# Performance work log

Hardware: AMD Instinct MI355X
Metric: run time of the kernel (lower is better)

The kernel has to match this reference:

```python
import jax, jax.numpy as jnp
import numpy as np

B, M, NV, H, D = 32, 64, 65, 960, 480
ROUNDS = 5
SCALE = D ** -0.5


def _self_att(x, m, qw, qb):
    # x: [B, P, Q, C] attention over Q within each (b, p); m: [B, P, Q]
    qkv = x @ qw.T + qb                      # [B,P,Q,3C]
    q, k, v = jnp.split(qkv, 3, axis=-1)
    # torch builds mask@mask^T/C from a C-times repeated mask == outer product of mask values
    am = m[..., :, None] * m[..., None, :]   # [B,P,Q,Q]
    a = jnp.einsum('bpqc,bpkc->bpqk', q, k) * SCALE
    a = jnp.where(am == 0, -10000.0, a)
    a = jax.nn.softmax(a, axis=-1)
    return jnp.einsum('bpqk,bpkc->bpqc', a, v)


def _attn_logits(x, mask, qw, qb):
    # Attention_logits.forward: attend over value axis, then over key axis
    x = _self_att(x, mask, qw, qb)
    x = _self_att(jnp.swapaxes(x, 1, 2), jnp.swapaxes(mask, 1, 2), qw, qb)
    return jnp.swapaxes(x, 1, 2)


def _biaffine(x1, x2, W, lw, lb):
    # torch.nn.Bilinear (no bias) on the MxN outer grid + Linear(cat(x1,x2)) with bias,
    # computed without materializing the repeated [B,M,N,2D] tensor.
    d = x1.shape[-1]
    bil = jnp.einsum('bmi,oij,bnj->bmno', x1, W, x2)
    lin = (x1 @ lw[:, :d].T)[:, :, None, :] + (x2 @ lw[:, d:].T)[:, None, :, :] + lb
    return bil + lin


def _rounds(key, value, km, vm, W, lw, lb, fw, fb, qw, qb):
    # shared structure of type_classifier / single_classifier (rounds=5, max pooling)
    lm = km[:, :, None] * vm[:, None, :]     # [B,M,N]
    logits = None
    for i in range(ROUNDS):
        logits = _biaffine(key, value, W, lw, lb)          # [B,M,N,out]
        if i < ROUNDS - 1:
            logits = logits @ fw.T + fb                    # [B,M,N,D]
            logits = _attn_logits(logits, lm, qw, qb)
            key = key + logits.max(axis=2)                 # max-pool over values
            value = value + logits.max(axis=1)             # max-pool over keys
        else:
            logits = logits * lm[..., None]
    return logits


def setup_inputs() -> dict:
    root = jax.random.key(0)
    ks = list(jax.random.split(root, 40))
    it = iter(ks)
    nrm = lambda sh, s=0.02: (jax.random.normal(next(it), sh, jnp.float32) * s)
    key = jax.random.normal(next(it), (B, M, H), jnp.float32)
    value = jax.random.normal(next(it), (B, NV, H), jnp.float32)
    klen = jax.random.randint(next(it), (B,), 1, M + 1)
    key_mask = (jnp.arange(M)[None, :] < klen[:, None]).astype(jnp.float32)
    vlen = jax.random.randint(next(it), (B,), 1, NV + 1)
    value_mask = (jnp.arange(NV)[None, :] < vlen[:, None]).astype(jnp.float32)
    return dict(
        key=key, value=value, key_mask=key_mask, value_mask=value_mask,
        w_kt=nrm((D, H)), b_kt=nrm((D,)), w_vt=nrm((D, H)), b_vt=nrm((D,)),
        w_km=nrm((D, H)), b_km=nrm((D,)), w_vm=nrm((D, H)), b_vm=nrm((D,)),
        w_ks=nrm((D, H)), b_ks=nrm((D,)), w_vs=nrm((D, H)), b_vs=nrm((D,)),
        bt_W=nrm((3, D, D)), bt_lw=nrm((3, 2 * D)), bt_lb=nrm((3,)),
        bi_W=nrm((2, D, D)), bi_lw=nrm((2, 2 * D)), bi_lb=nrm((2,)),
        w_ffnt=nrm((D, 3)), b_ffnt=nrm((D,)), w_ffn=nrm((D, 2)), b_ffn=nrm((D,)),
        qkvt_w=nrm((3 * D, D)), qkvt_b=nrm((3 * D,)),
        qkv_w=nrm((3 * D, D)), qkv_b=nrm((3 * D,)),
        w_cls=nrm((2, 2 * D)), b_cls=nrm((2,)),
    )


def reference(key, value, key_mask, value_mask,
              w_kt, b_kt, w_vt, b_vt, w_km, b_km, w_vm, b_vm,
              w_ks, b_ks, w_vs, b_vs,
              bt_W, bt_lw, bt_lb, bi_W, bi_lw, bi_lb,
              w_ffnt, b_ffnt, w_ffn, b_ffn,
              qkvt_w, qkvt_b, qkv_w, qkv_b, w_cls, b_cls):
    # --- type classifier ---
    kt = key @ w_kt.T + b_kt
    vt = value @ w_vt.T + b_vt
    type_logits = _rounds(kt, vt, key_mask, value_mask,
                          bt_W, bt_lw, bt_lb, w_ffnt, b_ffnt, qkvt_w, qkvt_b)  # [B,M,NV,3]
    # drop type token from values
    v1 = value[:, 1:, :]
    vm1 = value_mask[:, 1:]
    type_token = jax.nn.softmax(type_logits[:, :, 0], axis=-1)   # [B,M,3]
    key_type = jnp.argmax(type_token, axis=-1)
    type_single = key_type == 1
    # --- multi classifier (masks unused, as in original) ---
    km_f = key @ w_km.T + b_km
    vm_f = v1 @ w_vm.T + b_vm
    multi_logits = ((km_f @ w_cls[:, :D].T)[:, :, None, :]
                    + (vm_f @ w_cls[:, D:].T)[:, None, :, :] + b_cls)  # [B,M,M? -> B,64,64,2]
    # --- single classifier with key mask restricted to single-link keys ---
    km2 = (key_mask.astype(bool) & type_single).astype(key_mask.dtype)
    ks_f = key @ w_ks.T + b_ks
    vs_f = v1 @ w_vs.T + b_vs
    single_logits = _rounds(ks_f, vs_f, km2, vm1,
                            bi_W, bi_lw, bi_lb, w_ffn, b_ffn, qkv_w, qkv_b)  # [B,64,64,2]
    return (type_logits, multi_logits, single_logits)
```

## Files before the change

kernel.cpp:

```cpp
#include <hip/hip_runtime.h>
#include <math.h>

constexpr int NB = 32;
constexpr int NM = 64;
constexpr int NNV = 65;
constexpr int NH = 960;
constexpr int ND = 480;
constexpr float ATT_SCALE = 0.045643546458763842f;

constexpr int OF_Pq = 0;
constexpr int OF_cq = 4320;
constexpr int OF_Q2 = 5760;
constexpr int OF_V2 = OF_Q2 + 2*1440;
constexpr int OF_dq = 10080;
constexpr int OF_dv = OF_dq + 2*480;
constexpr int OF_S  = 11520;
constexpr int OF_u  = 11529;
constexpr int OF_r  = 11532;
constexpr int OF_w  = 11535;
constexpr int FOLD_SZ = 11552;

typedef float f32x4 __attribute__((ext_vector_type(4)));
typedef short s16x8 __attribute__((ext_vector_type(8)));

__device__ __forceinline__ float wave_sum(float v) {
#pragma unroll
  for (int d = 32; d; d >>= 1) v += __shfl_xor(v, d);
  return v;
}

__device__ __forceinline__ void split_bf16(float x, short& hi, short& lo) {
  union { float f; unsigned u; } a; a.f = x;
  unsigned uh = a.u + 0x7fffu + ((a.u >> 16) & 1u);
  hi = (short)(uh >> 16);
  union { unsigned u; float f; } b; b.u = ((unsigned)(unsigned short)hi) << 16;
  union { float f; unsigned u; } c; c.f = x - b.f;
  unsigned ul = c.u + 0x7fffu + ((c.u >> 16) & 1u);
  lo = (short)(ul >> 16);
}

struct ProjCfg {
  const float* X; const float* W; const float* bias; float* C;
  int R; int x0; int rpb; int xbs;
};
struct Proj6 { ProjCfg c[6]; };

constexpr int KP = 40;

__global__ __launch_bounds__(256) void k_projM(Proj6 P, int K)
{
  __shared__ unsigned short As_hi[64][KP], As_lo[64][KP];
  __shared__ unsigned short Bs_hi[48][KP], Bs_lo[48][KP];
  int p = blockIdx.x, total = gridDim.x;
  int q = total >> 3, r = total & 7;
  int xk = p & 7, idx = p >> 3;
  int lgc = (xk < r) ? (xk * (q + 1) + idx) : (r * (q + 1) + (xk - r) * q + idx);
  int mp = lgc / 10, nx = lgc - mp * 10;
  ProjCfg cfg; int my;
  if      (mp < 32)  { cfg = P.c[0]; my = mp; }
  else if (mp < 65)  { cfg = P.c[1]; my = mp - 32; }
  else if (mp < 97)  { cfg = P.c[2]; my = mp - 65; }
  else if (mp < 129) { cfg = P.c[3]; my = mp - 97; }
  else if (mp < 161) { cfg = P.c[4]; my = mp - 129; }
  else               { cfg = P.c[5]; my = mp - 161; }
  const int m0 = my * 64, n0 = nx * 48;
  const int tid = threadIdx.x;
  const int l6 = tid & 63, w = tid >> 6;
  const int lr = tid >> 2, kc = (tid & 3) * 8;
  const float* Arow = nullptr;
  {
    int rr = m0 + lr;
    if (rr < cfg.R) {
      int b = rr / cfg.rpb, r2 = rr - b * cfg.rpb;
      Arow = cfg.X + (size_t)b * cfg.xbs + (size_t)(cfg.x0 + r2) * K;
    }
  }
  const float* Brow = (lr < 48) ? (cfg.W + (size_t)(n0 + lr) * K) : nullptr;
  const int fr = l6 & 15, fk = (l6 >> 4) * 8;
  f32x4 acc0 = {0.f, 0.f, 0.f, 0.f}, acc1 = acc0, acc2 = acc0;
  for (int k0 = 0; k0 < K; k0 += 32) {
    float xs[8] = {0.f, 0.f, 0.f, 0.f, 0.f, 0.f, 0.f, 0.f};
    if (Arow) {
      float4 a0 = *(const float4*)(Arow + k0 + kc);
      float4 a1 = *(const float4*)(Arow + k0 + kc + 4);
      xs[0] = a0.x; xs[1] = a0.y; xs[2] = a0.z; xs[3] = a0.w;
      xs[4] = a1.x; xs[5] = a1.y; xs[6] = a1.z; xs[7] = a1.w;
    }
    s16x8 vh, vl;
#pragma unroll
    for (int e = 0; e < 8; ++e) { short h, lo2; split_bf16(xs[e], h, lo2); vh[e] = h; vl[e] = lo2; }
    *(s16x8*)&As_hi[lr][kc] = vh;
    *(s16x8*)&As_lo[lr][kc] = vl;
    if (Brow) {
      float4 b0 = *(const float4*)(Brow + k0 + kc);
      float4 b1 = *(const float4*)(Brow + k0 + kc + 4);
      float ys[8] = {b0.x, b0.y, b0.z, b0.w, b1.x, b1.y, b1.z, b1.w};
      s16x8 wh, wl;
#pragma unroll
      for (int e = 0; e < 8; ++e) { short h, lo2; split_bf16(ys[e], h, lo2); wh[e] = h; wl[e] = lo2; }
      *(s16x8*)&Bs_hi[lr][kc] = wh;
      *(s16x8*)&Bs_lo[lr][kc] = wl;
    }
    __syncthreads();
    s16x8 ah = *(const s16x8*)&As_hi[16 * w + fr][fk];
    s16x8 al = *(const s16x8*)&As_lo[16 * w + fr][fk];
    {
      s16x8 bh = *(const s16x8*)&Bs_hi[fr][fk];
      s16x8 bl = *(const s16x8*)&Bs_lo[fr][fk];
      acc0 = __builtin_amdgcn_mfma_f32_16x16x32_bf16(ah, bh, acc0, 0, 0, 0);
      acc0 = __builtin_amdgcn_mfma_f32_16x16x32_bf16(ah, bl, acc0, 0, 0, 0);
      acc0 = __builtin_amdgcn_mfma_f32_16x16x32_bf16(al, bh, acc0, 0, 0, 0);
    }
    {
      s16x8 bh = *(const s16x8*)&Bs_hi[16 + fr][fk];
      s16x8 bl = *(const s16x8*)&Bs_lo[16 + fr][fk];
      acc1 = __builtin_amdgcn_mfma_f32_16x16x32_bf16(ah, bh, acc1, 0, 0, 0);
      acc1 = __builtin_amdgcn_mfma_f32_16x16x32_bf16(ah, bl, acc1, 0, 0, 0);
      acc1 = __builtin_amdgcn_mfma_f32_16x16x32_bf16(al, bh, acc1, 0, 0, 0);
    }
    {
      s16x8 bh = *(const s16x8*)&Bs_hi[32 + fr][fk];
      s16x8 bl = *(const s16x8*)&Bs_lo[32 + fr][fk];
      acc2 = __builtin_amdgcn_mfma_f32_16x16x32_bf16(ah, bh, acc2, 0, 0, 0);
      acc2 = __builtin_amdgcn_mfma_f32_16x16x32_bf16(ah, bl, acc2, 0, 0, 0);
      acc2 = __builtin_amdgcn_mfma_f32_16x16x32_bf16(al, bh, acc2, 0, 0, 0);
    }
    __syncthreads();
  }
#pragma unroll
  for (int c = 0; c < 3; ++c) {
    f32x4 av = (c == 0) ? acc0 : (c == 1) ? acc1 : acc2;
    int n = n0 + 16 * c + fr;
    float bv = cfg.bias[n];
#pragma unroll
    for (int g = 0; g < 4; ++g) {
      int rr = m0 + 16 * w + (l6 >> 4) * 4 + g;
      if (rr < cfg.R) cfg.C[(size_t)rr * ND + n] = av[g] + bv;
    }
  }
}

__global__ __launch_bounds__(256) void k_tmpM(
    const float* __restrict__ Key, const float* __restrict__ W,
    float* __restrict__ T, int O)
{
  __shared__ unsigned short As_hi[64][KP], As_lo[64][KP];
  __shared__ unsigned short Bs_hi[48][KP], Bs_lo[48][KP];
  const int n0 = blockIdx.x * 48;
  const int o = blockIdx.y, b = blockIdx.z;
  const int tid = threadIdx.x;
  const int l6 = tid & 63, w = tid >> 6;
  const int lr = tid >> 2, kc = (tid & 3) * 8;
  const float* Arow = Key + (size_t)b * NM * ND + (size_t)lr * ND;
  const float* Wo = W + (size_t)o * ND * ND;
  const int fr = l6 & 15, fk = (l6 >> 4) * 8;
  f32x4 acc0 = {0.f, 0.f, 0.f, 0.f}, acc1 = acc0, acc2 = acc0;
  for (int k0 = 0; k0 < ND; k0 += 32) {
    {
      float4 a0 = *(const float4*)(Arow + k0 + kc);
      float4 a1 = *(const float4*)(Arow + k0 + kc + 4);
      float xs[8] = {a0.x, a0.y, a0.z, a0.w, a1.x, a1.y, a1.z, a1.w};
      s16x8 vh, vl;
#pragma unroll
      for (int e = 0; e < 8; ++e) { short h, lo2; split_bf16(xs[e], h, lo2); vh[e] = h; vl[e] = lo2; }
      *(s16x8*)&As_hi[lr][kc] = vh;
      *(s16x8*)&As_lo[lr][kc] = vl;
    }
    if (lr < 48) {
      s16x8 wh, wl;
#pragma unroll
      for (int e = 0; e < 8; ++e) {
        float x = Wo[(size_t)(k0 + kc + e) * ND + n0 + lr];
        short h, lo2; split_bf16(x, h, lo2); wh[e] = h; wl[e] = lo2;
      }
      *(s16x8*)&Bs_hi[lr][kc] = wh;
      *(s16x8*)&Bs_lo[lr][kc] = wl;
    }
    __syncthreads();
    s16x8 ah = *(const s16x8*)&As_hi[16 * w + fr][fk];
    s16x8 al = *(const s16x8*)&As_lo[16 * w + fr][fk];
    {
      s16x8 bh = *(const s16x8*)&Bs_hi[fr][fk];
      s16x8 bl = *(const s16x8*)&Bs_lo[fr][fk];
      acc0 = __builtin_amdgcn_mfma_f32_16x16x32_bf16(ah, bh, acc0, 0, 0, 0);
      acc0 = __builtin_amdgcn_mfma_f32_16x16x32_bf16(ah, bl, acc0, 0, 0, 0);
      acc0 = __builtin_amdgcn_mfma_f32_16x16x32_bf16(al, bh, acc0, 0, 0, 0);
    }
    {
      s16x8 bh = *(const s16x8*)&Bs_hi[16 + fr][fk];
      s16x8 bl = *(const s16x8*)&Bs_lo[16 + fr][fk];
      acc1 = __builtin_amdgcn_mfma_f32_16x16x32_bf16(ah, bh, acc1, 0, 0, 0);
      acc1 = __builtin_amdgcn_mfma_f32_16x16x32_bf16(ah, bl, acc1, 0, 0, 0);
      acc1 = __builtin_amdgcn_mfma_f32_16x16x32_bf16(al, bh, acc1, 0, 0, 0);
    }
    {
      s16x8 bh = *(const s16x8*)&Bs_hi[32 + fr][fk];
      s16x8 bl = *(const s16x8*)&Bs_lo[32 + fr][fk];
      acc2 = __builtin_amdgcn_mfma_f32_16x16x32_bf16(ah, bh, acc2, 0, 0, 0);
      acc2 = __builtin_amdgcn_mfma_f32_16x16x32_bf16(ah, bl, acc2, 0, 0, 0);
      acc2 = __builtin_amdgcn_mfma_f32_16x16x32_bf16(al, bh, acc2, 0, 0, 0);
    }
    __syncthreads();
  }
  float* C = T + ((size_t)(b * O + o) * NM) * ND;
#pragma unroll
  for (int c = 0; c < 3; ++c) {
    f32x4 av = (c == 0) ? acc0 : (c == 1) ? acc1 : acc2;
    int n = n0 + 16 * c + fr;
#pragma unroll
    for (int g = 0; g < 4; ++g) {
      int rr = 16 * w + (l6 >> 4) * 4 + g;
      C[(size_t)rr * ND + n] = av[g];
    }
  }
}

template <int O, int NVX>
__global__ __launch_bounds__(256) void k_bilatt0(
    const float* __restrict__ T, const float* __restrict__ Val,
    const float* __restrict__ linK, const float* __restrict__ linV,
    const float* __restrict__ lb, const float* __restrict__ F,
    const float* __restrict__ km, const float* __restrict__ vm,
    int vmOff, int vmStride, float* __restrict__ Y1)
{
  __shared__ float Ls[NVX][3];
  __shared__ float STs[NVX][3];
  __shared__ float hs[NVX], gs[NVX], mkj[NVX];
  __shared__ float Pm[NVX][66];
  __shared__ float rmx[NVX][3];
  __shared__ float rsum[NVX][3];
  __shared__ float ry[NVX][3][3];
  __shared__ float lvs[NVX][3];
  const int b = blockIdx.x >> 6, m = blockIdx.x & 63;
  const int tid = threadIdx.x;
  const int lane = tid & 63, w = tid >> 6;

  for (int j = tid; j < NVX; j += 256) {
    mkj[j] = vm[b * vmStride + vmOff + j];
#pragma unroll
    for (int o = 0; o < O; ++o) lvs[j][o] = linV[((size_t)b * NVX + j) * O + o];
  }
  float4 tsr[O][2];
#pragma unroll
  for (int o = 0; o < O; ++o) {
    const float4* trow = (const float4*)(T + (((size_t)b * O + o) * NM + m) * (size_t)ND);
    tsr[o][0] = trow[lane];
    tsr[o][1] = (lane < 56) ? trow[64 + lane] : make_float4(0.f, 0.f, 0.f, 0.f);
  }
  float lk[O];
#pragma unroll
  for (int o = 0; o < O; ++o) lk[o] = linK[((size_t)b * NM + m) * O + o] + lb[o];
  const float gm = km[b * NM + m];
  const bool gz = (gm == 0.f);

  for (int n = w; n < NVX; n += 4) {
    const float4* vrow = (const float4*)(Val + ((size_t)b * NVX + n) * (size_t)ND);
    float4 v0 = vrow[lane];
    float4 v1 = (lane < 56) ? vrow[64 + lane] : make_float4(0.f, 0.f, 0.f, 0.f);
    float a[3] = {0.f, 0.f, 0.f};
#pragma unroll
    for (int o = 0; o < O; ++o) {
      a[o] = v0.x * tsr[o][0].x + v0.y * tsr[o][0].y + v0.z * tsr[o][0].z + v0.w * tsr[o][0].w
           + v1.x * tsr[o][1].x + v1.y * tsr[o][1].y + v1.z * tsr[o][1].z + v1.w * tsr[o][1].w;
    }
#pragma unroll
    for (int o = 0; o < O; ++o) a[o] = wave_sum(a[o]);
    if (lane == 0) {
#pragma unroll
      for (int o = 0; o < O; ++o) Ls[n][o] = a[o] + lk[o] + lvs[n][o];
      if (O == 2) Ls[n][2] = 0.f;
    }
  }
  __syncthreads();
  const float* Sm = F + OF_S;
  const float u0 = F[OF_u], u1 = F[OF_u + 1], u2 = F[OF_u + 2];
  const float r0 = F[OF_r], r1 = F[OF_r + 1], r2 = F[OF_r + 2];
  const float wc = F[OF_w];
  if (tid < NVX) {
    int j = tid;
    float t0 = Ls[j][0], t1 = Ls[j][1], t2 = Ls[j][2];
    STs[j][0] = t0 * Sm[0] + t1 * Sm[3] + t2 * Sm[6];
    STs[j][1] = t0 * Sm[1] + t1 * Sm[4] + t2 * Sm[7];
    STs[j][2] = t0 * Sm[2] + t1 * Sm[5] + t2 * Sm[8];
    hs[j] = t0 * u0 + t1 * u1 + t2 * u2;
    gs[j] = t0 * r0 + t1 * r1 + t2 * r2;
  }
  __syncthreads();
  const bool act = tid < NVX * 3;
  int i = 0, qq = 0, jlo = 0, jhi = 0;
  float st0 = 0, st1 = 0, st2 = 0, hi = 0;
  bool rowz = true;
  if (act) {
    i = tid / 3; qq = tid - i * 3;
    jlo = qq * 22; jhi = (jlo + 22 < NVX) ? jlo + 22 : NVX;
    st0 = STs[i][0]; st1 = STs[i][1]; st2 = STs[i][2]; hi = hs[i];
    rowz = gz || (mkj[i] == 0.f);
    float mx = -3.0e38f;
    for (int j = jlo; j < jhi; ++j) {
      float s = st0 * Ls[j][0] + st1 * Ls[j][1] + hi + gs[j] + wc;
      if (O == 3) s += st2 * Ls[j][2];
      s = (rowz || mkj[j] == 0.f) ? -10000.f : ATT_SCALE * s;
      Pm[i][j] = s;
      mx = fmaxf(mx, s);
    }
    rmx[i][qq] = mx;
  }
  __syncthreads();
  if (act) {
    float mx = fmaxf(fmaxf(rmx[i][0], rmx[i][1]), rmx[i][2]);
    float sum = 0.f, y0 = 0.f, y1 = 0.f, y2 = 0.f;
    for (int j = jlo; j < jhi; ++j) {
      float pp = __expf(Pm[i][j] - mx);
      sum += pp; y0 += pp * Ls[j][0]; y1 += pp * Ls[j][1];
      if (O == 3) y2 += pp * Ls[j][2];
    }
    rsum[i][qq] = sum; ry[i][qq][0] = y0; ry[i][qq][1] = y1; ry[i][qq][2] = y2;
  }
  __syncthreads();
  if (tid < NVX) {
    int ii = tid;
    float sum = rsum[ii][0] + rsum[ii][1] + rsum[ii][2];
    float y0 = ry[ii][0][0] + ry[ii][1][0] + ry[ii][2][0];
    float y1 = ry[ii][0][1] + ry[ii][1][1] + ry[ii][2][1];
    float y2 = ry[ii][0][2] + ry[ii][1][2] + ry[ii][2][2];
    float inv = 1.f / sum;
    size_t ob = (((size_t)b * NM + m) * NVX + ii) * O;
    Y1[ob + 0] = y0 * inv;
    Y1[ob + 1] = y1 * inv;
    if (O == 3) Y1[ob + 2] = y2 * inv;
  }
}

template <int O, int NVX>
__global__ __launch_bounds__(256) void k_att1vupd(
    const float* __restrict__ Y1, float* __restrict__ Y2,
    const float* __restrict__ F,
    const float* __restrict__ km, const float* __restrict__ vm,
    int vmOff, int vmStride,
    float* __restrict__ valb, const float* __restrict__ lw,
    float* __restrict__ linV)
{
  __shared__ float Ys1[NM][3];
  __shared__ float STs[NM][3];
  __shared__ float hs[NM], gs[NM], mkm[NM];
  __shared__ float Pm[NM][66];
  __shared__ float rmx[NM][3];
  __shared__ float rsum[NM][3];
  __shared__ float ry[NM][3][3];
  __shared__ float Ys2[NM][3];
  __shared__ float vrow[ND];
  const int b = blockIdx.x / NVX, n = blockIdx.x - b * NVX;
  const int tid = threadIdx.x;
  for (int u = tid; u < NM * O; u += 256) {
    int mm = u % NM, o = u / NM;
    Ys1[mm][o] = Y1[(((size_t)b * NM + mm) * NVX + n) * O + o];
  }
  if (tid < NM) {
    mkm[tid] = km[b * NM + tid];
    if (O == 2) Ys1[tid][2] = 0.f;
  }
  const float gm = vm[b * vmStride + vmOff + n];
  const bool gz = (gm == 0.f);
  __syncthreads();
  const float* Sm = F + OF_S + 16;
  const float u0 = F[OF_u + 16], u1 = F[OF_u + 17], u2 = F[OF_u + 18];
  const float r0 = F[OF_r + 16], r1 = F[OF_r + 17], r2 = F[OF_r + 18];
  const float wc = F[OF_w + 16];
  if (tid < NM) {
    int j = tid;
    float t0 = Ys1[j][0], t1 = Ys1[j][1], t2 = Ys1[j][2];
    STs[j][0] = t0 * Sm[0] + t1 * Sm[3] + t2 * Sm[6];
    STs[j][1] = t0 * Sm[1] + t1 * Sm[4] + t2 * Sm[7];
    STs[j][2] = t0 * Sm[2] + t1 * Sm[5] + t2 * Sm[8];
    hs[j] = t0 * u0 + t1 * u1 + t2 * u2;
    gs[j] = t0 * r0 + t1 * r1 + t2 * r2;
  }
  __syncthreads();
  const bool act = tid < NM * 3;
  int i = 0, qq = 0, jlo = 0, jhi = 0;
  float st0 = 0, st1 = 0, st2 = 0, hi = 0;
  bool rowz = true;
// ... 37 lines not shown
    if (O == 3) Y2[ob + 2] = y2;
    Ys2[ii][0] = y0; Ys2[ii][1] = y1; Ys2[ii][2] = (O == 3) ? y2 : 0.f;
  }
  __syncthreads();
  const float* V2 = F + OF_V2;
  const float* dv = F + OF_dv;
  for (int d = tid; d < ND; d += 256) {
    float v0 = V2[d], v1 = V2[ND + d], v2 = (O == 3) ? V2[2 * ND + d] : 0.f;
    float mx = -3.0e38f;
    for (int j = 0; j < NM; ++j) {
      float s = Ys2[j][0] * v0 + Ys2[j][1] * v1;
      if (O == 3) s += Ys2[j][2] * v2;
      mx = fmaxf(mx, s);
    }
    size_t di = ((size_t)b * NVX + n) * ND + d;
    float nv = valb[di] + mx + dv[d];
    valb[di] = nv;
    vrow[d] = nv;
  }
  __syncthreads();
  const int wv = tid >> 6, lane = tid & 63;
  if (wv < O) {
    float acc = 0.f;
    for (int d = lane; d < ND; d += 64) acc += vrow[d] * lw[(size_t)wv * 2 * ND + ND + d];
    acc = wave_sum(acc);
    if (lane == 0) linV[((size_t)b * NVX + n) * O + wv] = acc;
  }
}

template <int O, int NVX>
__global__ __launch_bounds__(256) void k_kupd(
    const float* __restrict__ Y2, const float* __restrict__ F,
    float* __restrict__ keyb, const float* __restrict__ lw,
    float* __restrict__ linK)
{
  __shared__ float Ys[NVX][3];
  __shared__ float krow[ND];
  const int b = blockIdx.x >> 6, m = blockIdx.x & 63;
  const int tid = threadIdx.x;
  for (int u = tid; u < NVX * O; u += 256) {
    int j = u % NVX, o = u / NVX;
    Ys[j][o] = Y2[(((size_t)b * NVX + j) * NM + m) * O + o];
  }
  __syncthreads();
  const float* V2 = F + OF_V2;
  const float* dv = F + OF_dv;
  for (int d = tid; d < ND; d += 256) {
    float v0 = V2[d], v1 = V2[ND + d], v2 = (O == 3) ? V2[2 * ND + d] : 0.f;
    float mx = -3.0e38f;
    for (int j = 0; j < NVX; ++j) {
      float s = Ys[j][0] * v0 + Ys[j][1] * v1;
      if (O == 3) s += Ys[j][2] * v2;
      mx = fmaxf(mx, s);
    }
    size_t di = ((size_t)b * NM + m) * ND + d;
    float nv = keyb[di] + mx + dv[d];
    keyb[di] = nv;
    krow[d] = nv;
  }
  __syncthreads();
  const int wv = tid >> 6, lane = tid & 63;
  if (wv < O) {
    float acc = 0.f;
    for (int d = lane; d < ND; d += 64) acc += krow[d] * lw[(size_t)wv * 2 * ND + d];
    acc = wave_sum(acc);
    if (lane == 0) linK[((size_t)b * NM + m) * O + wv] = acc;
  }
}

template <int O, int NVX>
__global__ __launch_bounds__(256) void k_bilfin(
    const float* __restrict__ T, const float* __restrict__ Val,
    const float* __restrict__ linK, const float* __restrict__ linV,
    const float* __restrict__ lb, const float* __restrict__ km,
    const float* __restrict__ vm, int vmOff, int vmStride,
    float* __restrict__ Out)
{
  const int b = blockIdx.x >> 6, m = blockIdx.x & 63;
  const int tid = threadIdx.x;
  const int lane = tid & 63, w = tid >> 6;
  float4 tsr[O][2];
#pragma unroll
  for (int o = 0; o < O; ++o) {
    const float4* trow = (const float4*)(T + (((size_t)b * O + o) * NM + m) * (size_t)ND);
    tsr[o][0] = trow[lane];
    tsr[o][1] = (lane < 56) ? trow[64 + lane] : make_float4(0.f, 0.f, 0.f, 0.f);
  }
  float lk[O];
#pragma unroll
  for (int o = 0; o < O; ++o) lk[o] = linK[((size_t)b * NM + m) * O + o] + lb[o];
  const float kmv = km[b * NM + m];
  for (int n = w; n < NVX; n += 4) {
    const float4* vrow = (const float4*)(Val + ((size_t)b * NVX + n) * (size_t)ND);
    float4 v0 = vrow[lane];
    float4 v1 = (lane < 56) ? vrow[64 + lane] : make_float4(0.f, 0.f, 0.f, 0.f);
    float a[3] = {0.f, 0.f, 0.f};
#pragma unroll
    for (int o = 0; o < O; ++o) {
      a[o] = v0.x * tsr[o][0].x + v0.y * tsr[o][0].y + v0.z * tsr[o][0].z + v0.w * tsr[o][0].w
           + v1.x * tsr[o][1].x + v1.y * tsr[o][1].y + v1.z * tsr[o][1].z + v1.w * tsr[o][1].w;
    }
#pragma unroll
    for (int o = 0; o < O; ++o) a[o] = wave_sum(a[o]);
    if (lane == 0) {
      float msk = kmv * vm[b * vmStride + vmOff + n];
      size_t ob = (((size_t)b * NM + m) * NVX + n) * O;
#pragma unroll
      for (int o = 0; o < O; ++o)
        Out[ob + o] = (a[o] + lk[o] + linV[((size_t)b * NVX + n) * O + o]) * msk;
    }
  }
}

struct SpCfg { const float* X; const float* W; float* Out; int R; int O; int wStride; int wOff; };
__global__ __launch_bounds__(256) void k_sproj6(
    SpCfg s0, SpCfg s1, SpCfg s2, SpCfg s3, SpCfg s4, SpCfg s5)
{
  int z = blockIdx.y;
  SpCfg c = (z == 0) ? s0 : (z == 1) ? s1 : (z == 2) ? s2 : (z == 3) ? s3 : (z == 4) ? s4 : s5;
  int gid = blockIdx.x * 4 + (threadIdx.x >> 6);
  if (gid >= c.R * c.O) return;
  int lane = threadIdx.x & 63;
  int r = gid / c.O, o = gid - r * c.O;
  const float* x = c.X + (size_t)r * ND;
  const float* wp = c.W + (size_t)o * c.wStride + c.wOff;
  float acc = 0.f;
  for (int d = lane; d < ND; d += 64) acc += x[d] * wp[d];
  acc = wave_sum(acc);
  if (lane == 0) c.Out[gid] = acc;
}

struct FoldCfg { const float* fw; const float* fb; const float* qw; const float* qb; float* F; int O; };

__global__ __launch_bounds__(256) void k_fold1B(FoldCfg A, FoldCfg Bc)
{
  FoldCfg c = (blockIdx.y == 0) ? A : Bc;
  int O = c.O;
  int gid = blockIdx.x * 4 + (threadIdx.x >> 6);
  int lane = threadIdx.x & 63;
  if (gid >= 3 * ND) return;
  int part = gid / ND, cc0 = gid - part * ND;
  const float* qrow = c.qw + (size_t)(part * ND + cc0) * ND;
  float p0 = 0.f, p1 = 0.f, p2 = 0.f, cc = 0.f;
// ... 107 lines not shown
  }
}

__global__ void k_type(const float* __restrict__ tl, const float* __restrict__ key_mask,
                       float* __restrict__ km2)
{
  int i = blockIdx.x * blockDim.x + threadIdx.x;
  if (i >= NB * NM) return;
  const float* p = tl + (size_t)i * NNV * 3;
  float l0 = p[0], l1 = p[1], l2 = p[2];
  int arg = 0;
  float best = l0;
  if (l1 > best) { best = l1; arg = 1; }
  if (l2 > best) { best = l2; arg = 2; }
  km2[i] = (key_mask[i] != 0.f && arg == 1) ? 1.f : 0.f;
}

__global__ void k_multi(const float* __restrict__ a, const float* __restrict__ bb,
                        const float* __restrict__ bc, float* __restrict__ out)
{
  int i = blockIdx.x * blockDim.x + threadIdx.x;
  if (i >= NB * NM * NM * 2) return;
  int c = i & 1;
  int t = i >> 1;
  int n = t % NM; t /= NM;
  int m = t % NM;
  int b = t / NM;
  out[i] = a[((size_t)b * NM + m) * 2 + c] + bb[((size_t)b * NM + n) * 2 + c] + bc[c];
}

template <int O, int NVX>
static void run_rounds(hipStream_t stream,
                       float* keyb, float* valb,
                       const float* kmp, const float* vmp, int vmOff, int vmStride,
                       const float* Wb, const float* lwp, const float* lbp,
                       float* fold, float* linK, float* linV,
                       float* tmp, float* Y1, float* Y2, float* outp)
{
  dim3 blk(256);
  for (int r = 0; r < 5; ++r) {
    k_tmpM<<<dim3(10, O, NB), blk, 0, stream>>>(keyb, Wb, tmp, O);
    if (r < 4) {
      k_bilatt0<O, NVX><<<dim3(NB * NM), blk, 0, stream>>>(
          tmp, valb, linK, linV, lbp, fold, kmp, vmp, vmOff, vmStride, Y1);
      k_att1vupd<O, NVX><<<dim3(NB * NVX), blk, 0, stream>>>(
          Y1, Y2, fold, kmp, vmp, vmOff, vmStride, valb, lwp, linV);
      k_kupd<O, NVX><<<dim3(NB * NM), blk, 0, stream>>>(Y2, fold, keyb, lwp, linK);
    } else {
      k_bilfin<O, NVX><<<dim3(NB * NM), blk, 0, stream>>>(
          tmp, valb, linK, linV, lbp, kmp, vmp, vmOff, vmStride, outp);
    }
  }
}

extern "C" void kernel_launch(void* const* d_in, const int* in_sizes, int n_in,
                              void* d_out, int out_size, void* d_ws, size_t ws_size,
                              hipStream_t stream)
{
  const float* key        = (const float*)d_in[0];
  const float* value      = (const float*)d_in[1];
  const float* key_mask   = (const float*)d_in[2];
  const float* value_mask = (const float*)d_in[3];
  const float* w_kt = (const float*)d_in[4];  const float* b_kt = (const float*)d_in[5];
  const float* w_vt = (const float*)d_in[6];  const float* b_vt = (const float*)d_in[7];
  const float* w_km = (const float*)d_in[8];  const float* b_km = (const float*)d_in[9];
  const float* w_vm = (const float*)d_in[10]; const float* b_vm = (const float*)d_in[11];
  const float* w_ks = (const float*)d_in[12]; const float* b_ks = (const float*)d_in[13];
  const float* w_vs = (const float*)d_in[14]; const float* b_vs = (const float*)d_in[15];
  const float* bt_W = (const float*)d_in[16]; const float* bt_lw = (const float*)d_in[17];
  const float* bt_lb = (const float*)d_in[18];
  const float* bi_W = (const float*)d_in[19]; const float* bi_lw = (const float*)d_in[20];
  const float* bi_lb = (const float*)d_in[21];
  const float* w_ffnt = (const float*)d_in[22]; const float* b_ffnt = (const float*)d_in[23];
  const float* w_ffn  = (const float*)d_in[24]; const float* b_ffn  = (const float*)d_in[25];
  const float* qkvt_w = (const float*)d_in[26]; const float* qkvt_b = (const float*)d_in[27];
  const float* qkv_w  = (const float*)d_in[28]; const float* qkv_b  = (const float*)d_in[29];
  const float* w_cls  = (const float*)d_in[30]; const float* b_cls  = (const float*)d_in[31];

  float* ws = (float*)d_ws;
  size_t off = 0;
  float* kt_t  = ws + off; off += (size_t)NB * NM * ND;
  float* vt_t  = ws + off; off += (size_t)NB * NNV * ND;
  float* kt_s  = ws + off; off += (size_t)NB * NM * ND;
  float* vt_s  = ws + off; off += (size_t)NB * NM * ND;
  float* tmp   = ws + off; off += (size_t)NB * 3 * NM * ND;
  float* Y1    = ws + off; off += (size_t)NB * NM * NNV * 3;
  float* Y2    = ws + off; off += (size_t)NB * NM * NNV * 3;
  float* linK_t = ws + off; off += (size_t)NB * NM * 3;
  float* linV_t = ws + off; off += (size_t)NB * NNV * 3;
  float* linK_s = ws + off; off += (size_t)NB * NM * 3;
  float* linV_s = ws + off; off += (size_t)NB * NM * 3;
  float* fold_t = ws + off; off += FOLD_SZ;
  float* fold_s = ws + off; off += FOLD_SZ;
  float* km2   = ws + off; off += (size_t)NB * NM;
  float* a2    = ws + off; off += (size_t)NB * NM * 2;
  float* b2    = ws + off; off += (size_t)NB * NM * 2;
  (void)off; (void)ws_size; (void)in_sizes; (void)n_in; (void)out_size;

  float* kmf = tmp;
  float* vmf = tmp + (size_t)NB * NM * ND;

  float* out_type   = (float*)d_out;
  float* out_multi  = out_type + (size_t)NB * NM * NNV * 3;
  float* out_single = out_multi + (size_t)NB * NM * NM * 2;

  dim3 blk(256);

  Proj6 P;
  P.c[0] = { key,   w_kt, b_kt, kt_t, NB * NM,  0, NM,  NM * NH };
  P.c[1] = { value, w_vt, b_vt, vt_t, NB * NNV, 0, NNV, NNV * NH };
  P.c[2] = { key,   w_ks, b_ks, kt_s, NB * NM,  0, NM,  NM * NH };
  P.c[3] = { value, w_vs, b_vs, vt_s, NB * NM,  1, NM,  NNV * NH };
  P.c[4] = { key,   w_km, b_km, kmf,  NB * NM,  0, NM,  NM * NH };
  P.c[5] = { value, w_vm, b_vm, vmf,  NB * NM,  1, NM,  NNV * NH };
  k_projM<<<dim3(193 * 10), blk, 0, stream>>>(P, NH);

  FoldCfg ft = { w_ffnt, b_ffnt, qkvt_w, qkvt_b, fold_t, 3 };
  FoldCfg fs = { w_ffn,  b_ffn,  qkv_w,  qkv_b,  fold_s, 2 };
  k_fold1B<<<dim3(360, 2), blk, 0, stream>>>(ft, fs);
  k_fold2B<<<dim3(364, 2), blk, 0, stream>>>(ft, fs);
  k_fold3B<<<dim3(4, 2), blk, 0, stream>>>(ft, fs);

  SpCfg s0 = { kt_t, bt_lw, linK_t, NB * NM,  3, 2 * ND, 0 };
  SpCfg s1 = { vt_t, bt_lw, linV_t, NB * NNV, 3, 2 * ND, ND };
  SpCfg s2 = { kt_s, bi_lw, linK_s, NB * NM,  2, 2 * ND, 0 };
  SpCfg s3 = { vt_s, bi_lw, linV_s, NB * NM,  2, 2 * ND, ND };
  SpCfg s4 = { kmf,  w_cls, a2,     NB * NM,  2, 2 * ND, 0 };
  SpCfg s5 = { vmf,  w_cls, b2,     NB * NM,  2, 2 * ND, ND };
  k_sproj6<<<dim3((NB * NNV * 3 + 3) / 4, 6), blk, 0, stream>>>(s0, s1, s2, s3, s4, s5);

  k_multi<<<dim3((NB * NM * NM * 2 + 255) / 256), blk, 0, stream>>>(a2, b2, b_cls, out_multi);

  run_rounds<3, NNV>(stream, kt_t, vt_t, key_mask, value_mask, 0, NNV,
                     bt_W, bt_lw, bt_lb, fold_t, linK_t, linV_t,
                     tmp, Y1, Y2, out_type);

  k_type<<<dim3(8), blk, 0, stream>>>(out_type, key_mask, km2);

  run_rounds<2, NM>(stream, kt_s, vt_s, km2, value_mask, 1, NNV,
                    bi_W, bi_lw, bi_lb, fold_s, linK_s, linV_s,
                    tmp, Y1, Y2, out_single);
}
```

Before: 1.097 ms.

## Pre-split weights and keys into bf16 hi/lo buffers; restructure bilinear dot kernels

Adds conversion kernels that split the projection weights and transposed biaffine weights into bf16 hi/lo arrays once per call. The GEMM kernels then load the pre-split operands directly instead of re-splitting fp32 on every tile, which also removes the strided transposed weight reads in k_tmpM. k_kupd now writes hi/lo copies of the updated key. The bilinear logit kernels stage T and value chunks in shared memory, with one thread per (n,o) output instead of wave reductions. The cost is extra launches, conversion traffic and workspace, plus heavier shared-memory use in the attention kernels.

```diff
diff --git a/kernel.cpp b/kernel.cpp
--- a/kernel.cpp
+++ b/kernel.cpp
@@ -20,6 +20,7 @@
 constexpr int OF_w  = 11535;
 constexpr int FOLD_SZ = 11552;
 
+typedef unsigned short u16;
 typedef float f32x4 __attribute__((ext_vector_type(4)));
 typedef short s16x8 __attribute__((ext_vector_type(8)));
 
@@ -39,8 +40,54 @@
   lo = (short)(ul >> 16);
 }
 
+struct CvtN { const float* s[6]; u16* h[6]; u16* l[6]; int n4[6]; };
+__global__ __launch_bounds__(256) void k_cvtN(CvtN C)
+{
+  int z = blockIdx.y;
+  const float* src = C.s[z];
+  u16* dh = C.h[z]; u16* dl = C.l[z];
+  int n4 = C.n4[z];
+  for (int i = blockIdx.x * 256 + threadIdx.x; i < n4; i += gridDim.x * 256) {
+    float4 v = ((const float4*)src)[i];
+    short h0, l0, h1, l1, h2, l2, h3, l3;
+    split_bf16(v.x, h0, l0); split_bf16(v.y, h1, l1);
+    split_bf16(v.z, h2, l2); split_bf16(v.w, h3, l3);
+    s16x8 dummy;
+    ushort4 hv, lv;
+    hv.x = (u16)h0; hv.y = (u16)h1; hv.z = (u16)h2; hv.w = (u16)h3;
+    lv.x = (u16)l0; lv.y = (u16)l1; lv.z = (u16)l2; lv.w = (u16)l3;
+    ((ushort4*)dh)[i] = hv;
+    ((ushort4*)dl)[i] = lv;
+    (void)dummy;
+  }
+}
+
+__global__ __launch_bounds__(256) void k_cvtT(
+    const float* __restrict__ btW, const float* __restrict__ biW,
+    u16* __restrict__ wtHi, u16* __restrict__ wtLo)
+{
+  __shared__ float s[32][33];
+  const int z = blockIdx.z;
+  const float* src = (z < 3) ? (btW + (size_t)z * ND * ND) : (biW + (size_t)(z - 3) * ND * ND);
+  u16* dh = wtHi + (size_t)z * ND * ND;
+  u16* dl = wtLo + (size_t)z * ND * ND;
+  const int k0 = blockIdx.y * 32, n0 = blockIdx.x * 32;
+  const int tx = threadIdx.x & 31, ty = threadIdx.x >> 5;
+#pragma unroll
+  for (int q = 0; q < 4; ++q)
+    s[ty + q * 8][tx] = src[(size_t)(k0 + ty + q * 8) * ND + n0 + tx];
+  __syncthreads();
+#pragma unroll
+  for (int q = 0; q < 4; ++q) {
+    float v = s[tx][ty + q * 8];
+    short h, l; split_bf16(v, h, l);
+    size_t di = (size_t)(n0 + ty + q * 8) * ND + k0 + tx;
+    dh[di] = (u16)h; dl[di] = (u16)l;
+  }
+}
+
 struct ProjCfg {
-  const float* X; const float* W; const float* bias; float* C;
+  const float* X; const u16* Whi; const u16* Wlo; const float* bias; float* C;
   int R; int x0; int rpb; int xbs;
 };
 struct Proj6 { ProjCfg c[6]; };
@@ -49,8 +96,8 @@
 
 __global__ __launch_bounds__(256) void k_projM(Proj6 P, int K)
 {
-  __shared__ unsigned short As_hi[64][KP], As_lo[64][KP];
-  __shared__ unsigned short Bs_hi[48][KP], Bs_lo[48][KP];
+  __shared__ u16 As_hi[64][KP], As_lo[64][KP];
+  __shared__ u16 Bs_hi[48][KP], Bs_lo[48][KP];
   int p = blockIdx.x, total = gridDim.x;
   int q = total >> 3, r = total & 7;
   int xk = p & 7, idx = p >> 3;
@@ -75,7 +122,11 @@
       Arow = cfg.X + (size_t)b * cfg.xbs + (size_t)(cfg.x0 + r2) * K;
     }
   }
-  const float* Brow = (lr < 48) ? (cfg.W + (size_t)(n0 + lr) * K) : nullptr;
+  const u16* Bhi = nullptr; const u16* Blo = nullptr;
+  if (lr < 48) {
+    size_t off = (size_t)(n0 + lr) * K;
+    Bhi = cfg.Whi + off; Blo = cfg.Wlo + off;
+  }
   const int fr = l6 & 15, fk = (l6 >> 4) * 8;
   f32x4 acc0 = {0.f, 0.f, 0.f, 0.f}, acc1 = acc0, acc2 = acc0;
   for (int k0 = 0; k0 < K; k0 += 32) {
@@ -91,15 +142,9 @@
     for (int e = 0; e < 8; ++e) { short h, lo2; split_bf16(xs[e], h, lo2); vh[e] = h; vl[e] = lo2; }
     *(s16x8*)&As_hi[lr][kc] = vh;
     *(s16x8*)&As_lo[lr][kc] = vl;
-    if (Brow) {
-      float4 b0 = *(const float4*)(Brow + k0 + kc);
-      float4 b1 = *(const float4*)(Brow + k0 + kc + 4);
-      float ys[8] = {b0.x, b0.y, b0.z, b0.w, b1.x, b1.y, b1.z, b1.w};
-      s16x8 wh, wl;
-#pragma unroll
-      for (int e = 0; e < 8; ++e) { short h, lo2; split_bf16(ys[e], h, lo2); wh[e] = h; wl[e] = lo2; }
-      *(s16x8*)&Bs_hi[lr][kc] = wh;
-      *(s16x8*)&Bs_lo[lr][kc] = wl;
+    if (Bhi) {
+      *(s16x8*)&Bs_hi[lr][kc] = *(const s16x8*)(Bhi + k0 + kc);
+      *(s16x8*)&Bs_lo[lr][kc] = *(const s16x8*)(Blo + k0 + kc);
     }
     __syncthreads();
     s16x8 ah = *(const s16x8*)&As_hi[16 * w + fr][fk];
@@ -141,40 +186,28 @@
 }
 
 __global__ __launch_bounds__(256) void k_tmpM(
-    const float* __restrict__ Key, const float* __restrict__ W,
+    const u16* __restrict__ Khi, const u16* __restrict__ Klo,
+    const u16* __restrict__ Wthi, const u16* __restrict__ Wtlo,
     float* __restrict__ T, int O)
 {
-  __shared__ unsigned short As_hi[64][KP], As_lo[64][KP];
-  __shared__ unsigned short Bs_hi[48][KP], Bs_lo[48][KP];
+  __shared__ u16 As_hi[64][KP], As_lo[64][KP];
+  __shared__ u16 Bs_hi[48][KP], Bs_lo[48][KP];
   const int n0 = blockIdx.x * 48;
   const int o = blockIdx.y, b = blockIdx.z;
   const int tid = threadIdx.x;
   const int l6 = tid & 63, w = tid >> 6;
   const int lr = tid >> 2, kc = (tid & 3) * 8;
-  const float* Arow = Key + (size_t)b * NM * ND + (size_t)lr * ND;
-  const float* Wo = W + (size_t)o * ND * ND;
+  const size_t aoff = ((size_t)b * NM + lr) * ND;
+  const size_t boff = ((size_t)o * ND + n0 + lr) * ND;
+  const bool bok = lr < 48;
   const int fr = l6 & 15, fk = (l6 >> 4) * 8;
   f32x4 acc0 = {0.f, 0.f, 0.f, 0.f}, acc1 = acc0, acc2 = acc0;
   for (int k0 = 0; k0 < ND; k0 += 32) {
-    {
-      float4 a0 = *(const float4*)(Arow + k0 + kc);
-      float4 a1 = *(const float4*)(Arow + k0 + kc + 4);
-      float xs[8] = {a0.x, a0.y, a0.z, a0.w, a1.x, a1.y, a1.z, a1.w};
-      s16x8 vh, vl;
-#pragma unroll
-      for (int e = 0; e < 8; ++e) { short h, lo2; split_bf16(xs[e], h, lo2); vh[e] = h; vl[e] = lo2; }
-      *(s16x8*)&As_hi[lr][kc] = vh;
-      *(s16x8*)&As_lo[lr][kc] = vl;
-    }
-    if (lr < 48) {
-      s16x8 wh, wl;
-#pragma unroll
-      for (int e = 0; e < 8; ++e) {
-        float x = Wo[(size_t)(k0 + kc + e) * ND + n0 + lr];
-        short h, lo2; split_bf16(x, h, lo2); wh[e] = h; wl[e] = lo2;
-      }
-      *(s16x8*)&Bs_hi[lr][kc] = wh;
-      *(s16x8*)&Bs_lo[lr][kc] = wl;
+    *(s16x8*)&As_hi[lr][kc] = *(const s16x8*)(Khi + aoff + k0 + kc);
+    *(s16x8*)&As_lo[lr][kc] = *(const s16x8*)(Klo + aoff + k0 + kc);
+    if (bok) {
+      *(s16x8*)&Bs_hi[lr][kc] = *(const s16x8*)(Wthi + boff + k0 + kc);
+      *(s16x8*)&Bs_lo[lr][kc] = *(const s16x8*)(Wtlo + boff + k0 + kc);
     }
     __syncthreads();
     s16x8 ah = *(const s16x8*)&As_hi[16 * w + fr][fk];
@@ -223,53 +256,47 @@
     const float* __restrict__ km, const float* __restrict__ vm,
     int vmOff, int vmStride, float* __restrict__ Y1)
 {
+  __shared__ float ts[O][ND];
+  __shared__ float buf[NVX][97];
   __shared__ float Ls[NVX][3];
   __shared__ float STs[NVX][3];
   __shared__ float hs[NVX], gs[NVX], mkj[NVX];
-  __shared__ float Pm[NVX][66];
-  __shared__ float rmx[NVX][3];
-  __shared__ float rsum[NVX][3];
-  __shared__ float ry[NVX][3][3];
+  __shared__ float rmx[NVX][3], rsum[NVX][3], ry[NVX][3][3];
   __shared__ float lvs[NVX][3];
   const int b = blockIdx.x >> 6, m = blockIdx.x & 63;
   const int tid = threadIdx.x;
-  const int lane = tid & 63, w = tid >> 6;
-
+  for (int idx = tid; idx < O * ND; idx += 256) {
+    int o = idx / ND, d = idx - o * ND;
+    ts[o][d] = T[(((size_t)b * O + o) * NM + m) * ND + d];
+  }
   for (int j = tid; j < NVX; j += 256) {
     mkj[j] = vm[b * vmStride + vmOff + j];
 #pragma unroll
     for (int o = 0; o < O; ++o) lvs[j][o] = linV[((size_t)b * NVX + j) * O + o];
   }
-  float4 tsr[O][2];
-#pragma unroll
-  for (int o = 0; o < O; ++o) {
-    const float4* trow = (const float4*)(T + (((size_t)b * O + o) * NM + m) * (size_t)ND);
-    tsr[o][0] = trow[lane];
-    tsr[o][1] = (lane < 56) ? trow[64 + lane] : make_float4(0.f, 0.f, 0.f, 0.f);
-  }
-  float lk[O];
-#pragma unroll
-  for (int o = 0; o < O; ++o) lk[o] = linK[((size_t)b * NM + m) * O + o] + lb[o];
   const float gm = km[b * NM + m];
   const bool gz = (gm == 0.f);
-
-  for (int n = w; n < NVX; n += 4) {
-    const float4* vrow = (const float4*)(Val + ((size_t)b * NVX + n) * (size_t)ND);
-    float4 v0 = vrow[lane];
-    float4 v1 = (lane < 56) ? vrow[64 + lane] : make_float4(0.f, 0.f, 0.f, 0.f);
-    float a[3] = {0.f, 0.f, 0.f};
-#pragma unroll
-    for (int o = 0; o < O; ++o) {
-      a[o] = v0.x * tsr[o][0].x + v0.y * tsr[o][0].y + v0.z * tsr[o][0].z + v0.w * tsr[o][0].w
-           + v1.x * tsr[o][1].x + v1.y * tsr[o][1].y + v1.z * tsr[o][1].z + v1.w * tsr[o][1].w;
-    }
-#pragma unroll
-    for (int o = 0; o < O; ++o) a[o] = wave_sum(a[o]);
-    if (lane == 0) {
-#pragma unroll
-      for (int o = 0; o < O; ++o) Ls[n][o] = a[o] + lk[o] + lvs[n][o];
-      if (O == 2) Ls[n][2] = 0.f;
-    }
+  const bool act1 = tid < NVX * O;
+  const int an = act1 ? (tid % NVX) : 0;
+  const int ao = act1 ? (tid / NVX) : 0;
+  float acc = 0.f;
+  for (int c = 0; c < 5; ++c) {
+    const int d0 = c * 96;
+    __syncthreads();
+    for (int u = tid; u < NVX * 24; u += 256) {
+      int n = u / 24, f = (u - n * 24) * 4;
+      float4 v = *(const float4*)(Val + ((size_t)b * NVX + n) * ND + d0 + f);
+      buf[n][f + 0] = v.x; buf[n][f + 1] = v.y; buf[n][f + 2] = v.z; buf[n][f + 3] = v.w;
+    }
+    __syncthreads();
+    if (act1) {
+      const float* tp = &ts[ao][d0];
+#pragma unroll 8
+      for (int dd = 0; dd < 96; ++dd) acc += buf[an][dd] * tp[dd];
+    }
+  }
+  if (act1) {
+    Ls[an][ao] = acc + linK[((size_t)b * NM + m) * O + ao] + lvs[an][ao] + lb[ao];
   }
   __syncthreads();
   const float* Sm = F + OF_S;
@@ -278,7 +305,7 @@
   const float wc = F[OF_w];
   if (tid < NVX) {
     int j = tid;
-    float t0 = Ls[j][0], t1 = Ls[j][1], t2 = Ls[j][2];
+    float t0 = Ls[j][0], t1 = Ls[j][1], t2 = (O == 3) ? Ls[j][2] : 0.f;
     STs[j][0] = t0 * Sm[0] + t1 * Sm[3] + t2 * Sm[6];
     STs[j][1] = t0 * Sm[1] + t1 * Sm[4] + t2 * Sm[7];
     STs[j][2] = t0 * Sm[2] + t1 * Sm[5] + t2 * Sm[8];
@@ -300,7 +327,7 @@
       float s = st0 * Ls[j][0] + st1 * Ls[j][1] + hi + gs[j] + wc;
       if (O == 3) s += st2 * Ls[j][2];
       s = (rowz || mkj[j] == 0.f) ? -10000.f : ATT_SCALE * s;
-      Pm[i][j] = s;
+      buf[i][j] = s;
       mx = fmaxf(mx, s);
     }
     rmx[i][qq] = mx;
@@ -310,7 +337,7 @@
     float mx = fmaxf(fmaxf(rmx[i][0], rmx[i][1]), rmx[i][2]);
     float sum = 0.f, y0 = 0.f, y1 = 0.f, y2 = 0.f;
     for (int j = jlo; j < jhi; ++j) {
-      float pp = __expf(Pm[i][j] - mx);
+      float pp = __expf(buf[i][j] - mx);
       sum += pp; y0 += pp * Ls[j][0]; y1 += pp * Ls[j][1];
       if (O == 3) y2 += pp * Ls[j][2];
     }
@@ -344,9 +371,7 @@
   __shared__ float STs[NM][3];
   __shared__ float hs[NM], gs[NM], mkm[NM];
   __shared__ float Pm[NM][66];
-  __shared__ float rmx[NM][3];
-  __shared__ float rsum[NM][3];
-  __shared__ float ry[NM][3][3];
+  __shared__ float rmx[NM][3], rsum[NM][3], ry[NM][3][3];
   __shared__ float Ys2[NM][3];
   __shared__ float vrow[ND];
   const int b = blockIdx.x / NVX, n = blockIdx.x - b * NVX;
@@ -450,7 +475,7 @@
 __global__ __launch_bounds__(256) void k_kupd(
     const float* __restrict__ Y2, const float* __restrict__ F,
     float* __restrict__ keyb, const float* __restrict__ lw,
-    float* __restrict__ linK)
+    float* __restrict__ linK, u16* __restrict__ kbHi, u16* __restrict__ kbLo)
 {
   __shared__ float Ys[NVX][3];
   __shared__ float krow[ND];
@@ -463,6 +488,7 @@
   __syncthreads();
   const float* V2 = F + OF_V2;
   const float* dv = F + OF_dv;
+  const size_t rowb = ((size_t)b * NM + m) * ND;
   for (int d = tid; d < ND; d += 256) {
     float v0 = V2[d], v1 = V2[ND + d], v2 = (O == 3) ? V2[2 * ND + d] : 0.f;
     float mx = -3.0e38f;
@@ -471,10 +497,11 @@
       if (O == 3) s += Ys[j][2] * v2;
       mx = fmaxf(mx, s);
     }
-    size_t di = ((size_t)b * NM + m) * ND + d;
-    float nv = keyb[di] + mx + dv[d];
-    keyb[di] = nv;
+    float nv = keyb[rowb + d] + mx + dv[d];
+    keyb[rowb + d] = nv;
     krow[d] = nv;
+    short h, l; split_bf16(nv, h, l);
+    kbHi[rowb + d] = (u16)h; kbLo[rowb + d] = (u16)l;
   }
   __syncthreads();
   const int wv = tid >> 6, lane = tid & 63;
@@ -494,39 +521,38 @@
     const float* __restrict__ vm, int vmOff, int vmStride,
     float* __restrict__ Out)
 {
+  __shared__ float ts[O][ND];
+  __shared__ float buf[NVX][97];
   const int b = blockIdx.x >> 6, m = blockIdx.x & 63;
   const int tid = threadIdx.x;
-  const int lane = tid & 63, w = tid >> 6;
-  float4 tsr[O][2];
-#pragma unroll
-  for (int o = 0; o < O; ++o) {
-    const float4* trow = (const float4*)(T + (((size_t)b * O + o) * NM + m) * (size_t)ND);
-    tsr[o][0] = trow[lane];
-    tsr[o][1] = (lane < 56) ? trow[64 + lane] : make_float4(0.f, 0.f, 0.f, 0.f);
-  }
-  float lk[O];
-#pragma unroll
-  for (int o = 0; o < O; ++o) lk[o] = linK[((size_t)b * NM + m) * O + o] + lb[o];
-  const float kmv = km[b * NM + m];
-  for (int n = w; n < NVX; n += 4) {
-    const float4* vrow = (const float4*)(Val + ((size_t)b * NVX + n) * (size_t)ND);
-    float4 v0 = vrow[lane];
-    float4 v1 = (lane < 56) ? vrow[64 + lane] : make_float4(0.f, 0.f, 0.f, 0.f);
-    float a[3] = {0.f, 0.f, 0.f};
-#pragma unroll
-    for (int o = 0; o < O; ++o) {
-      a[o] = v0.x * tsr[o][0].x + v0.y * tsr[o][0].y + v0.z * tsr[o][0].z + v0.w * tsr[o][0].w
-           + v1.x * tsr[o][1].x + v1.y * tsr[o][1].y + v1.z * tsr[o][1].z + v1.w * tsr[o][1].w;
-    }
-#pragma unroll
-    for (int o = 0; o < O; ++o) a[o] = wave_sum(a[o]);
-    if (lane == 0) {
-      float msk = kmv * vm[b * vmStride + vmOff + n];
-      size_t ob = (((size_t)b * NM + m) * NVX + n) * O;
-#pragma unroll
-      for (int o = 0; o < O; ++o)
-        Out[ob + o] = (a[o] + lk[o] + linV[((size_t)b * NVX + n) * O + o]) * msk;
-    }
+  for (int idx = tid; idx < O * ND; idx += 256) {
+    int o = idx / ND, d = idx - o * ND;
+    ts[o][d] = T[(((size_t)b * O + o) * NM + m) * ND + d];
+  }
+  const bool act1 = tid < NVX * O;
+  const int an = act1 ? (tid % NVX) : 0;
+  const int ao = act1 ? (tid / NVX) : 0;
+  float acc = 0.f;
+  for (int c = 0; c < 5; ++c) {
+    const int d0 = c * 96;
+    __syncthreads();
+    for (int u = tid; u < NVX * 24; u += 256) {
+      int n = u / 24, f = (u - n * 24) * 4;
+      float4 v = *(const float4*)(Val + ((size_t)b * NVX + n) * ND + d0 + f);
+      buf[n][f + 0] = v.x; buf[n][f + 1] = v.y; buf[n][f + 2] = v.z; buf[n][f + 3] = v.w;
+    }
+    __syncthreads();
+    if (act1) {
+      const float* tp = &ts[ao][d0];
+#pragma unroll 8
+      for (int dd = 0; dd < 96; ++dd) acc += buf[an][dd] * tp[dd];
+    }
+  }
+  if (act1) {
+    float msk = km[b * NM + m] * vm[b * vmStride + vmOff + an];
+    Out[(((size_t)b * NM + m) * NVX + an) * O + ao] =
+        (acc + linK[((size_t)b * NM + m) * O + ao]
+             + linV[((size_t)b * NVX + an) * O + ao] + lb[ao]) * msk;
   }
 }
 
@@ -700,20 +726,22 @@
 template <int O, int NVX>
 static void run_rounds(hipStream_t stream,
                        float* keyb, float* valb,
+                       u16* ktHi, u16* ktLo,
+                       const u16* wtHi, const u16* wtLo,
                        const float* kmp, const float* vmp, int vmOff, int vmStride,
-                       const float* Wb, const float* lwp, const float* lbp,
+                       const float* lwp, const float* lbp,
                        float* fold, float* linK, float* linV,
                        float* tmp, float* Y1, float* Y2, float* outp)
 {
   dim3 blk(256);
   for (int r = 0; r < 5; ++r) {
-    k_tmpM<<<dim3(10, O, NB), blk, 0, stream>>>(keyb, Wb, tmp, O);
+    k_tmpM<<<dim3(10, O, NB), blk, 0, stream>>>(ktHi, ktLo, wtHi, wtLo, tmp, O);
     if (r < 4) {
       k_bilatt0<O, NVX><<<dim3(NB * NM), blk, 0, stream>>>(
           tmp, valb, linK, linV, lbp, fold, kmp, vmp, vmOff, vmStride, Y1);
       k_att1vupd<O, NVX><<<dim3(NB * NVX), blk, 0, stream>>>(
           Y1, Y2, fold, kmp, vmp, vmOff, vmStride, valb, lwp, linV);
-      k_kupd<O, NVX><<<dim3(NB * NM), blk, 0, stream>>>(Y2, fold, keyb, lwp, linK);
+      k_kupd<O, NVX><<<dim3(NB * NM), blk, 0, stream>>>(Y2, fold, keyb, lwp, linK, ktHi, ktLo);
     } else {
       k_bilfin<O, NVX><<<dim3(NB * NM), blk, 0, stream>>>(
           tmp, valb, linK, linV, lbp, kmp, vmp, vmOff, vmStride, outp);
@@ -747,23 +775,33 @@
 
   float* ws = (float*)d_ws;
   size_t off = 0;
-  float* kt_t  = ws + off; off += (size_t)NB * NM * ND;
-  float* vt_t  = ws + off; off += (size_t)NB * NNV * ND;
-  float* kt_s  = ws + off; off += (size_t)NB * NM * ND;
-  float* vt_s  = ws + off; off += (size_t)NB * NM * ND;
-  float* tmp   = ws + off; off += (size_t)NB * 3 * NM * ND;
-  float* Y1    = ws + off; off += (size_t)NB * NM * NNV * 3;
-  float* Y2    = ws + off; off += (size_t)NB * NM * NNV * 3;
-  float* linK_t = ws + off; off += (size_t)NB * NM * 3;
-  float* linV_t = ws + off; off += (size_t)NB * NNV * 3;
-  float* linK_s = ws + off; off += (size_t)NB * NM * 3;
-  float* linV_s = ws + off; off += (size_t)NB * NM * 3;
-  float* fold_t = ws + off; off += FOLD_SZ;
-  float* fold_s = ws + off; off += FOLD_SZ;
-  float* km2   = ws + off; off += (size_t)NB * NM;
-  float* a2    = ws + off; off += (size_t)NB * NM * 2;
-  float* b2    = ws + off; off += (size_t)NB * NM * 2;
-  (void)off; (void)ws_size; (void)in_sizes; (void)n_in; (void)out_size;
+  auto alloc = [&](size_t nfloat) { float* p = ws + off; off += (nfloat + 3) & ~(size_t)3; return p; };
+
+  float* kt_t   = alloc((size_t)NB * NM * ND);
+  float* vt_t   = alloc((size_t)NB * NNV * ND);
+  float* kt_s   = alloc((size_t)NB * NM * ND);
+  float* vt_s   = alloc((size_t)NB * NM * ND);
+  float* tmp    = alloc((size_t)NB * 3 * NM * ND);
+  float* Y1     = alloc((size_t)NB * NM * NNV * 3);
+  float* Y2     = alloc((size_t)NB * NM * NNV * 3);
+  float* linK_t = alloc((size_t)NB * NM * 3);
+  float* linV_t = alloc((size_t)NB * NNV * 3);
+  float* linK_s = alloc((size_t)NB * NM * 3);
+  float* linV_s = alloc((size_t)NB * NM * 3);
+  float* fold_t = alloc(FOLD_SZ);
+  float* fold_s = alloc(FOLD_SZ);
+  float* km2    = alloc((size_t)NB * NM);
+  float* a2     = alloc((size_t)NB * NM * 2);
+  float* b2     = alloc((size_t)NB * NM * 2);
+  u16* WPhi  = (u16*)alloc((size_t)6 * ND * NH / 2);
+  u16* WPlo  = (u16*)alloc((size_t)6 * ND * NH / 2);
+  u16* WtPhi = (u16*)alloc((size_t)5 * ND * ND / 2);
+  u16* WtPlo = (u16*)alloc((size_t)5 * ND * ND / 2);
+  u16* ktHi_t = (u16*)alloc((size_t)NB * NM * ND / 2);
+  u16* ktLo_t = (u16*)alloc((size_t)NB * NM * ND / 2);
+  u16* ktHi_s = (u16*)alloc((size_t)NB * NM * ND / 2);
+  u16* ktLo_s = (u16*)alloc((size_t)NB * NM * ND / 2);
+  (void)ws_size; (void)in_sizes; (void)n_in; (void)out_size;
 
   float* kmf = tmp;
   float* vmf = tmp + (size_t)NB * NM * ND;
@@ -774,14 +812,32 @@
 
   dim3 blk(256);
 
+  const float* wsrc[6] = { w_kt, w_vt, w_ks, w_vs, w_km, w_vm };
+  CvtN cw;
+  for (int i = 0; i < 6; ++i) {
+    cw.s[i] = wsrc[i];
+    cw.h[i] = WPhi + (size_t)i * ND * NH;
+    cw.l[i] = WPlo + (size_t)i * ND * NH;
+    cw.n4[i] = ND * NH / 4;
+  }
+  k_cvtN<<<dim3(512, 6), blk, 0, stream>>>(cw);
+
+  k_cvtT<<<dim3(15, 15, 5), blk, 0, stream>>>(bt_W, bi_W, WtPhi, WtPlo);
+
   Proj6 P;
-  P.c[0] = { key,   w_kt, b_kt, kt_t, NB * NM,  0, NM,  NM * NH };
-  P.c[1] = { value, w_vt, b_vt, vt_t, NB * NNV, 0, NNV, NNV * NH };
-  P.c[2] = { key,   w_ks, b_ks, kt_s, NB * NM,  0, NM,  NM * NH };
-  P.c[3] = { value, w_vs, b_vs, vt_s, NB * NM,  1, NM,  NNV * NH };
-  P.c[4] = { key,   w_km, b_km, kmf,  NB * NM,  0, NM,  NM * NH };
-  P.c[5] = { value, w_vm, b_vm, vmf,  NB * NM,  1, NM,  NNV * NH };
+  P.c[0] = { key,   WPhi + 0*(size_t)ND*NH, WPlo + 0*(size_t)ND*NH, b_kt, kt_t, NB * NM,  0, NM,  NM * NH };
+  P.c[1] = { value, WPhi + 1*(size_t)ND*NH, WPlo + 1*(size_t)ND*NH, b_vt, vt_t, NB * NNV, 0, NNV, NNV * NH };
+  P.c[2] = { key,   WPhi + 2*(size_t)ND*NH, WPlo + 2*(size_t)ND*NH, b_ks, kt_s, NB * NM,  0, NM,  NM * NH };
+  P.c[3] = { value, WPhi + 3*(size_t)ND*NH, WPlo + 3*(size_t)ND*NH, b_vs, vt_s, NB * NM,  1, NM,  NNV * NH };
+  P.c[4] = { key,   WPhi + 4*(size_t)ND*NH, WPlo + 4*(size_t)ND*NH, b_km, kmf,  NB * NM,  0, NM,  NM * NH };
+  P.c[5] = { value, WPhi + 5*(size_t)ND*NH, WPlo + 5*(size_t)ND*NH, b_vm, vmf,  NB * NM,  1, NM,  NNV * NH };
   k_projM<<<dim3(193 * 10), blk, 0, stream>>>(P, NH);
+
+  CvtN ck;
+  ck.s[0] = kt_t; ck.h[0] = ktHi_t; ck.l[0] = ktLo_t; ck.n4[0] = NB * NM * ND / 4;
+  ck.s[1] = kt_s; ck.h[1] = ktHi_s; ck.l[1] = ktLo_s; ck.n4[1] = NB * NM * ND / 4;
+  for (int i = 2; i < 6; ++i) { ck.s[i] = kt_t; ck.h[i] = ktHi_t; ck.l[i] = ktLo_t; ck.n4[i] = 0; }
+  k_cvtN<<<dim3(512, 2), blk, 0, stream>>>(ck);
 
   FoldCfg ft = { w_ffnt, b_ffnt, qkvt_w, qkvt_b, fold_t, 3 };
   FoldCfg fs = { w_ffn,  b_ffn,  qkv_w,  qkv_b,  fold_s, 2 };
@@ -799,13 +855,16 @@
 
   k_multi<<<dim3((NB * NM * NM * 2 + 255) / 256), blk, 0, stream>>>(a2, b2, b_cls, out_multi);
 
-  run_rounds<3, NNV>(stream, kt_t, vt_t, key_mask, value_mask, 0, NNV,
-                     bt_W, bt_lw, bt_lb, fold_t, linK_t, linV_t,
+  run_rounds<3, NNV>(stream, kt_t, vt_t, ktHi_t, ktLo_t, WtPhi, WtPlo,
+                     key_mask, value_mask, 0, NNV,
+                     bt_lw, bt_lb, fold_t, linK_t, linV_t,
                      tmp, Y1, Y2, out_type);
 
   k_type<<<dim3(8), blk, 0, stream>>>(out_type, key_mask, km2);
 
-  run_rounds<2, NM>(stream, kt_s, vt_s, km2, value_mask, 1, NNV,
-                    bi_W, bi_lw, bi_lb, fold_s, linK_s, linV_s,
+  run_rounds<2, NM>(stream, kt_s, vt_s, ktHi_s, ktLo_s,
+                    WtPhi + (size_t)3 * ND * ND, WtPlo + (size_t)3 * ND * ND,
+                    km2, value_mask, 1, NNV,
+                    bi_lw, bi_lb, fold_s, linK_s, linV_s,
                     tmp, Y1, Y2, out_single);
 }
```

Measured after the change: 1.181 ms. 1.08x slower.
